# Kernel optimization log

Measured on AMD Instinct MI355X. Metric: run time of the kernel, lower is better.

Reference implementation:

```python
import jax, jax.numpy as jnp
import numpy as np

N, E, G = 50000, 800000, 128          # nodes, edges, graphs in batch
DF, DE, DT = 128, 256, 18             # dim_features, dim_embedding, dim_target
NUM_LAYERS = 4


def setup_inputs() -> dict:
    key = jax.random.key(0)
    ks = jax.random.split(key, 32)
    inp = {}
    inp["x"] = jax.random.normal(ks[0], (N, DF), jnp.float32)
    inp["edge_index"] = jax.random.randint(ks[1], (2, E), 0, N, dtype=jnp.int64)
    inp["batch"] = jnp.sort(jax.random.randint(ks[2], (N,), 0, G, dtype=jnp.int64))
    i = 3
    for l in range(NUM_LAYERS):
        din = DF if l == 0 else DE
        inp[f"Wl{l}"] = jax.random.normal(ks[i], (din, DE), jnp.float32) * (din ** -0.5); i += 1
        inp[f"bl{l}"] = jnp.zeros((DE,), jnp.float32)
        inp[f"Wr{l}"] = jax.random.normal(ks[i], (din, DE), jnp.float32) * (din ** -0.5); i += 1
        inp[f"Wm{l}"] = jax.random.normal(ks[i], (DE, DE), jnp.float32) * (DE ** -0.5); i += 1
        inp[f"bm{l}"] = jnp.zeros((DE,), jnp.float32)
    inp["fc1_W"] = jax.random.normal(ks[i], (NUM_LAYERS * DE, DE), jnp.float32) * ((NUM_LAYERS * DE) ** -0.5); i += 1
    inp["fc1_b"] = jnp.zeros((DE,), jnp.float32)
    inp["fc2_W"] = jax.random.normal(ks[i], (DE, DT), jnp.float32) * (DE ** -0.5); i += 1
    inp["fc2_b"] = jnp.zeros((DT,), jnp.float32)
    return inp


def _seg_max(v, idx, n):
    # scatter-max; empty segments -> 0 (PyG scatter 'max' convention)
    m = jax.ops.segment_max(v, idx, num_segments=n)
    return jnp.where(jnp.isfinite(m), m, 0.0)


def reference(x, edge_index, batch,
              Wl0, bl0, Wr0, Wm0, bm0,
              Wl1, bl1, Wr1, Wm1, bm1,
              Wl2, bl2, Wr2, Wm2, bm2,
              Wl3, bl3, Wr3, Wm3, bm3,
              fc1_W, fc1_b, fc2_W, fc2_b):
    src, dst = edge_index[0], edge_index[1]
    params = [(Wl0, bl0, Wr0, Wm0, bm0), (Wl1, bl1, Wr1, Wm1, bm1),
              (Wl2, bl2, Wr2, Wm2, bm2), (Wl3, bl3, Wr3, Wm3, bm3)]
    h = x
    outs = []
    for Wl, bl, Wr, Wm, bm in params:
        # SAGEConv(aggr='max'): lin_l(max_j x_j) + lin_r(x_i)
        agg = _seg_max(h[src], dst, h.shape[0])       # [N, din] gather + scatter-max
        h = agg @ Wl + bl + h @ Wr                    # [N, DE]
        h = jax.nn.relu(h @ Wm + bm)                  # fc_max + relu
        outs.append(h)
    hc = jnp.concatenate(outs, axis=1)                # [N, 4*DE]
    g = _seg_max(hc, batch, G)                        # global_max_pool -> [G, 4*DE]
    last_layer = jax.nn.relu(g @ fc1_W + fc1_b)       # [G, DE]
    out = last_layer @ fc2_W + fc2_b                  # [G, DT] (dropout = identity at eval)
    return jax.nn.log_softmax(out, axis=1), out, last_layer
```

## Files before the change

### kernel.cpp

```cpp
#include <hip/hip_runtime.h>
#include <stdint.h>

#define NN 50000
#define EE 800000
#define GG 128
#define DF 128
#define DE 256
#define NCHUNK ((NN + 255) / 256)

typedef unsigned short u16;
typedef __bf16 bf16x8 __attribute__((ext_vector_type(8)));
typedef float f32x4 __attribute__((ext_vector_type(4)));
typedef short s16x8 __attribute__((ext_vector_type(8)));

__device__ __forceinline__ float bf2f(u16 u) {
  union { unsigned int i; float f; } x; x.i = ((unsigned int)u) << 16; return x.f;
}
__device__ __forceinline__ u16 f2bf(float f) {
  union { float f; unsigned int i; } x; x.f = f;
  unsigned int i = x.i;
  return (u16)((i + 0x7fffu + ((i >> 16) & 1u)) >> 16);
}

__device__ __forceinline__ void async16(const void* g, void* l) {
  __builtin_amdgcn_global_load_lds(
      (const __attribute__((address_space(1))) void*)g,
      (__attribute__((address_space(3))) void*)l,
      16, 0, 0);
}

__device__ __forceinline__ s16x8 vmax8(s16x8 a, s16x8 b) {
  return __builtin_elementwise_max(a, b);
}

__global__ void detect_kernel(const u16* __restrict__ xr,
                              const unsigned* __restrict__ ei_words,
                              int* __restrict__ flags, int* __restrict__ counts) {
  int tid = threadIdx.x;
  if (blockIdx.x > 0) {
    int i = (blockIdx.x - 1) * 256 + tid;
    if (i < NN) counts[i] = 0;
    return;
  }
  __shared__ int red[2];
  if (tid < 2) red[tid] = 0;
  __syncthreads();
  int found = 0;
  for (int it = 0; it < 32; it++) {
    int i = it * 256 + tid;
    u16 a = xr[2 * i], b = xr[2 * i + 1];
    if (((a >> 7) & 0xFFu) == 0xFFu) found = 1;
    if (((b >> 7) & 0xFFu) == 0xFFu) found = 1;
  }
  if (__ballot(found)) { if ((tid & 63) == 0) atomicOr(&red[0], 1); }
  int nz = 0;
  if (tid < 128) {
    for (int j = 0; j < 4; j++) {
      unsigned w = ei_words[2 * (tid * 4 + j) + 1];
      if (w != 0u) nz = 1;
    }
  }
  if (__ballot(nz)) { if ((tid & 63) == 0) atomicOr(&red[1], 1); }
  __syncthreads();
  if (tid == 0) { flags[0] = red[0]; flags[1] = red[1]; }
}

__device__ __forceinline__ u16 ldw(const void* p, int idx, int f) {
  return f ? f2bf(((const float*)p)[idx]) : ((const u16*)p)[idx];
}

struct ConvSeg { const void* src; u16* dst; int start_blk; int n; };

struct PrepArgs {
  ConvSeg s[12]; int nseg; int conv_blocks;
  const void* x; u16* acat_x; u16* xk;
  const void* ei; const void* batch;
  int* src32; int* dst32; int* batch32; int* counts;
};

__global__ void prep_all(PrepArgs A, const int* __restrict__ flags) {
  int f = flags[0];
  int tid = threadIdx.x;
  int b = blockIdx.x;

  if (b < A.conv_blocks) {
    for (int i = 0; i < A.nseg; i++) {
      int nb = (A.s[i].n + 255) >> 8;
      if (b >= A.s[i].start_blk && b < A.s[i].start_blk + nb) {
        int idx = ((b - A.s[i].start_blk) << 8) + tid;
        if (idx < A.s[i].n) A.s[i].dst[idx] = ldw(A.s[i].src, idx, f);
        return;
      }
    }
    return;
  }
  b -= A.conv_blocks;

  if (b < 25000) {
    int i = b * 256 + tid;
    int node = i >> 7, d = i & 127;
    u16 v = ldw(A.x, i, f);
    A.acat_x[(long)node * 512 + d] = v;
    short s = (short)v;
    A.xk[i] = (u16)(s ^ ((s >> 15) & 0x7FFF));
    return;
  }
  b -= 25000;
  {
    int i64 = (flags[1] == 0);
    int i = b * 256 + tid;
    int s, d;
    if (i64) {
      s = (int)((const long long*)A.ei)[i];
      d = (int)((const long long*)A.ei)[EE + i];
    } else {
      s = ((const int*)A.ei)[i];
      d = ((const int*)A.ei)[EE + i];
    }
    s = min(max(s, 0), NN - 1);
    d = min(max(d, 0), NN - 1);
    A.src32[i] = s;
    A.dst32[i] = d;
    atomicAdd(&A.counts[d], 1);
    if (i < NN) {
      int bv = i64 ? (int)((const long long*)A.batch)[i] : ((const int*)A.batch)[i];
      A.batch32[i] = min(max(bv, 0), GG - 1);
    }
  }
}

struct TransArgs {
  const void* Wl[4]; const void* Wr[4]; const void* Wm[4]; const void* fc1W;
  u16* WcatT[4]; u16* WmT[4]; u16* fc1WT;
};

__global__ __launch_bounds__(256) void transpose_w(TransArgs T, const int* __restrict__ flags) {
  int f = flags[0];
  __shared__ u16 tile[64][65];
  int b = blockIdx.x;
  const void* src; u16* dst; int kt, ntile, Kd; int krow_off = 0;
  if (b < 16) {
    kt = b >> 2; ntile = b & 3; Kd = 256;
    if (kt * 64 < 128) { src = T.Wl[0]; } else { src = T.Wr[0]; krow_off = 128; }
    dst = T.WcatT[0];
  } else if (b < 112) {
    int l = 1 + (b - 16) / 32; int t = (b - 16) % 32;
    kt = t >> 2; ntile = t & 3; Kd = 512;
    if (kt * 64 < 256) { src = T.Wl[l]; } else { src = T.Wr[l]; krow_off = 256; }
    dst = T.WcatT[l];
  } else if (b < 176) {
    int l = (b - 112) / 16; int t = (b - 112) % 16;
    kt = t >> 2; ntile = t & 3; Kd = 256;
    src = T.Wm[l]; dst = T.WmT[l];
  } else {
    int t = b - 176;
    kt = t >> 2; ntile = t & 3; Kd = 1024;
    src = T.fc1W; dst = T.fc1WT;
  }
  int cj = threadIdx.x & 63, rp = threadIdx.x >> 6;
#pragma unroll 4
  for (int p = 0; p < 16; p++) {
    int krow = kt * 64 + p * 4 + rp;
    tile[p * 4 + rp][cj] = ldw(src, (krow - krow_off) * 256 + ntile * 64 + cj, f);
  }
  __syncthreads();
#pragma unroll 4
  for (int p = 0; p < 16; p++) {
    int nrow = ntile * 64 + p * 4 + rp;
    dst[(long)nrow * Kd + kt * 64 + cj] = tile[cj][p * 4 + rp];
  }
}

__global__ void rowptr_all(const int* __restrict__ counts, int* __restrict__ cursor,
                           int* __restrict__ row_ptr) {
  __shared__ int sh[256];
  int b = blockIdx.x, tid = threadIdx.x;
  int base = 0;
  for (int i = tid; i < b * 256; i += 256) base += counts[i];
  sh[tid] = base;
  __syncthreads();
  for (int off = 128; off > 0; off >>= 1) {
    if (tid < off) sh[tid] += sh[tid + off];
    __syncthreads();
  }
  base = sh[0];
  __syncthreads();
  int i = b * 256 + tid;
  int x = (i < NN) ? counts[i] : 0;
  sh[tid] = x;
  __syncthreads();
  for (int off = 1; off < 256; off <<= 1) {
    int v = (tid >= off) ? sh[tid - off] : 0;
    __syncthreads();
    sh[tid] += v;
    __syncthreads();
  }
  if (i < NN) {
    row_ptr[i + 1] = base + sh[tid];
    cursor[i] = base + sh[tid] - x;
  }
  if (i == 0) row_ptr[0] = 0;
}

__global__ void scatter_kernel(const int* __restrict__ srcA, const int* __restrict__ dstA,
                               int* __restrict__ cursor, int* __restrict__ col_src,
                               const int* __restrict__ batch, int* __restrict__ gs) {
  int e = blockIdx.x * blockDim.x + threadIdx.x;
  if (e < EE) {
    int slot = atomicAdd(&cursor[dstA[e]], 1);
    col_src[slot] = srcA[e];
  }
  if (blockIdx.x == 0 && threadIdx.x <= GG) {
    int g = threadIdx.x, lo = 0, hi = NN;
    while (lo < hi) { int mid = (lo + hi) >> 1; if (batch[mid] < g) lo = mid + 1; else hi = mid; }
    gs[g] = lo;
  }
}

template <int LPR, bool KEYED>
__global__ __launch_bounds__(256) void segmax_kernel(
    const u16* __restrict__ feat, int fstride,
    const int* __restrict__ row_ptr, const int* __restrict__ col_src,
    u16* __restrict__ agg_out, int ostride, int n) {
  constexpr int R = 64 / LPR;
  int node = blockIdx.x * 4 + (threadIdx.x >> 6);
  if (node >= n) return;
  int lane = threadIdx.x & 63;
  int sub = lane / LPR;
  int cp = lane % LPR;
  int beg = row_ptr[node], end = row_ptr[node + 1];
  s16x8 m = (s16x8)(short)(KEYED ? (short)0x807F : (short)0);
  const u16* fb = feat + cp * 8;

  int e = beg + sub;
  for (; e + 3 * R < end; e += 4 * R) {
    int s0 = col_src[e];
    int s1 = col_src[e + R];
    int s2 = col_src[e + 2 * R];
    int s3 = col_src[e + 3 * R];
    s16x8 v0 = *(const s16x8*)(fb + (long)s0 * fstride);
    s16x8 v1 = *(const s16x8*)(fb + (long)s1 * fstride);
    s16x8 v2 = *(const s16x8*)(fb + (long)s2 * fstride);
    s16x8 v3 = *(const s16x8*)(fb + (long)s3 * fstride);
    m = vmax8(m, vmax8(vmax8(v0, v1), vmax8(v2, v3)));
  }
  for (; e < end; e += R)
    m = vmax8(m, *(const s16x8*)(fb + (long)col_src[e] * fstride));

#pragma unroll
  for (int d = LPR; d < 64; d <<= 1) {
    union { s16x8 s; int i[4]; } t;
    t.s = m;
#pragma unroll
    for (int j = 0; j < 4; j++) t.i[j] = __shfl_xor(t.i[j], d);
    m = vmax8(m, t.s);
  }

  if (sub == 0) {
    if (KEYED) {
      if (beg == end) {
        m = (s16x8)(short)0;
      } else {
        s16x8 sp = (m >> 15) & (short)0x7FFF;
        m = m ^ sp;
      }
    }
    *(s16x8*)(agg_out + (long)node * ostride + cp * 8) = m;
  }
}

__global__ __launch_bounds__(512) void gemm256w(
    const u16* __restrict__ A, int lda, int K,
    const u16* __restrict__ BT,
    const u16* __restrict__ bias,
    u16* __restrict__ C, int ldc, int M, int relu_flag) {
  __shared__ u16 lsA[128 * 32];
  __shared__ u16 lsB[256 * 32];
  int tid = threadIdx.x;
  int lane = tid & 63, w = tid >> 6;
  int bm = blockIdx.x;
  int wm = (w & 1) << 6, wn = (w >> 1) << 6;
  int ln15 = lane & 15, quad = lane >> 4;

  f32x4 acc[4][4] = {};

  int r = tid >> 2;
  int c = (tid & 3) ^ (r & 3);
  const u16* gA = A + (long)min(bm * 128 + r, M - 1) * lda + c * 8;
  const u16* gB0 = BT + (long)r * K + c * 8;
  const u16* gB1 = BT + (long)(r + 128) * K + c * 8;
  u16* lA = lsA + w * 512;
  u16* lB0 = lsB + w * 512;
  u16* lB1 = lsB + 4096 + w * 512;
  int swz = (quad ^ (ln15 & 3)) << 3;

  for (int k0 = 0; k0 < K; k0 += 32) {
    async16(gA + k0, lA);
    async16(gB0 + k0, lB0);
    async16(gB1 + k0, lB1);
    __syncthreads();
    bf16x8 af[4], bfr[4];
#pragma unroll
    for (int t = 0; t < 4; t++) {
      af[t]  = *(const bf16x8*)(lsA + (wm + t * 16 + ln15) * 32 + swz);
      bfr[t] = *(const bf16x8*)(lsB + (wn + t * 16 + ln15) * 32 + swz);
    }
#pragma unroll
    for (int mt = 0; mt < 4; mt++)
#pragma unroll
      for (int nt = 0; nt < 4; nt++)
        acc[mt][nt] = __builtin_amdgcn_mfma_f32_16x16x32_bf16(af[mt], bfr[nt], acc[mt][nt], 0, 0, 0);
    __syncthreads();
  }

  float bv[4];
#pragma unroll
  for (int nt = 0; nt < 4; nt++)
    bv[nt] = bf2f(bias[wn + nt * 16 + ln15]);

#pragma unroll
  for (int mt = 0; mt < 4; mt++) {
    int row0 = bm * 128 + wm + mt * 16 + quad * 4;
#pragma unroll
    for (int rr = 0; rr < 4; rr++) {
      int row = row0 + rr;
      if (row < M) {
#pragma unroll
        for (int nt = 0; nt < 4; nt++) {
          float v = acc[mt][nt][rr] + bv[nt];
          if (relu_flag) v = fmaxf(v, 0.f);
          C[(long)row * ldc + wn + nt * 16 + ln15] = f2bf(v);
        }
      }
    }
  }
}

__global__ void pool_kernel(const u16* __restrict__ h, const int* __restrict__ gs,
                            u16* __restrict__ g_pool, int l) {
  int g = blockIdx.x;
  int chunk = threadIdx.x & 31;
  int rg = threadIdx.x >> 5;
  int beg = gs[g], end = gs[g + 1];
  s16x8 m = (s16x8)(short)0;
  const u16* hp = h + chunk * 8;
  for (int n = beg + rg; n < end; n += 32)
    m = vmax8(m, *(const s16x8*)(hp + (long)n * 512));
  __shared__ s16x8 red[32][32];
  red[rg][chunk] = m;
  __syncthreads();
  for (int s = 16; s >= 1; s >>= 1) {
    if (rg < s) red[rg][chunk] = vmax8(red[rg][chunk], red[rg + s][chunk]);
    __syncthreads();
  }
  if (rg == 0)
    *(s16x8*)(g_pool + g * 1024 + l * 256 + chunk * 8) = red[0][chunk];
}

__global__ __launch_bounds__(256) void fc1_gemm(
    const u16* __restrict__ A,
    const u16* __restrict__ BT,
    float* __restrict__ Cpart) {
  __shared__ u16 lsA[128 * 32];
  __shared__ u16 lsB[128 * 32];
  int tid = threadIdx.x;
  int lane = tid & 63, w = tid >> 6;
  int slice = blockIdx.x >> 1, bn = blockIdx.x & 1;
  int wm = (w & 1) << 6, wn = (w >> 1) << 6;
  int ln15 = lane & 15, quad = lane >> 4;

  f32x4 acc[4][4] = {};

  int cm = lane >> 2;
  int ck = (lane & 3) << 3;
  int kb = slice * 256;

  const u16* gA0 = A + (long)(w * 16 + cm) * 1024 + kb + ck;
  const u16* gA1 = A + (long)((w + 4) * 16 + cm) * 1024 + kb + ck;
  const u16* gB0 = BT + (long)(bn * 128 + w * 16 + cm) * 1024 + kb + ck;
  const u16* gB1 = BT + (long)(bn * 128 + (w + 4) * 16 + cm) * 1024 + kb + ck;
  u16* lA0 = lsA + w * 512;
  u16* lA1 = lsA + (w + 4) * 512;
  u16* lB0 = lsB + w * 512;
  u16* lB1 = lsB + (w + 4) * 512;

  for (int k0 = 0; k0 < 256; k0 += 32) {
    async16(gA0 + k0, lA0);
    async16(gA1 + k0, lA1);
    async16(gB0 + k0, lB0);
    async16(gB1 + k0, lB1);
    __syncthreads();
    bf16x8 af[4], bfr[4];
#pragma unroll
    for (int t = 0; t < 4; t++) {
      af[t]  = *(const bf16x8*)(lsA + (wm + t * 16 + ln15) * 32 + quad * 8);
      bfr[t] = *(const bf16x8*)(lsB + (wn + t * 16 + ln15) * 32 + quad * 8);
    }
#pragma unroll
    for (int mt = 0; mt < 4; mt++)
#pragma unroll
      for (int nt = 0; nt < 4; nt++)
        acc[mt][nt] = __builtin_amdgcn_mfma_f32_16x16x32_bf16(af[mt], bfr[nt], acc[mt][nt], 0, 0, 0);
    __syncthreads();
  }

  float* Cb = Cpart + slice * (GG * 256);
#pragma unroll
  for (int mt = 0; mt < 4; mt++) {
    int row0 = wm + mt * 16 + quad * 4;
#pragma unroll
    for (int r = 0; r < 4; r++)
#pragma unroll
      for (int nt = 0; nt < 4; nt++)
        Cb[(row0 + r) * 256 + bn * 128 + wn + nt * 16 + ln15] = acc[mt][nt][r];
  }
}

__global__ void fc2_head(const float* __restrict__ fc1part,
                         const u16* __restrict__ fc1b,
                         const u16* __restrict__ W,
                         const u16* __restrict__ b,
                         void* __restrict__ outbuf, const int* __restrict__ flags) {
  int g = blockIdx.x, t = threadIdx.x;
  __shared__ float lr[256];
  __shared__ float ps[144];
  __shared__ float sv[18];
  __shared__ float sred[2];
  float v = bf2f(fc1b[t]);
#pragma unroll
  for (int s = 0; s < 4; s++) v += fc1part[s * (GG * 256) + g * 256 + t];
  v = fmaxf(v, 0.f);
  lr[t] = v;
  if (flags[0]) ((float*)outbuf)[4608 + g * 256 + t] = v;
  else          ((u16*)outbuf)[4608 + g * 256 + t] = f2bf(v);
  __syncthreads();
  if (t < 144) {
    int o = t % 18, s = t / 18;
    float acc = 0.f;
    int k0 = s * 32;
#pragma unroll 8
    for (int k = k0; k < k0 + 32; k++)
      acc += lr[k] * bf2f(W[k * 18 + o]);
    ps[t] = acc;
  }
  __syncthreads();
  if (t < 18) {
    float acc = bf2f(b[t]);
#pragma unroll
    for (int s = 0; s < 8; s++) acc += ps[s * 18 + t];
    sv[t] = acc;
  }
  __syncthreads();
  if (t == 0) {
    float mx = sv[0];
    for (int i = 1; i < 18; i++) mx = fmaxf(mx, sv[i]);
    float s = 0.f;
    for (int i = 0; i < 18; i++) s += expf(sv[i] - mx);
    sred[0] = mx; sred[1] = logf(s);
  }
  __syncthreads();
  if (t < 18) {
    float raw = sv[t];
    float lsm = raw - sred[0] - sred[1];
    if (flags[0]) {
      ((float*)outbuf)[g * 18 + t] = lsm;
      ((float*)outbuf)[2304 + g * 18 + t] = raw;
    } else {
      ((u16*)outbuf)[g * 18 + t] = f2bf(lsm);
      ((u16*)outbuf)[2304 + g * 18 + t] = f2bf(raw);
    }
  }
}

extern "C" void kernel_launch(void* const* d_in, const int* in_sizes, int n_in,
                              void* d_out, int out_size, void* d_ws, size_t ws_size,
                              hipStream_t stream) {
  (void)in_sizes; (void)n_in; (void)out_size; (void)ws_size;
  const void* x = d_in[0];
  const void* ei = d_in[1];
  const void* batch = d_in[2];
  const void *Wl[4], *bl[4], *Wr[4], *Wm[4], *bm[4];
  for (int l = 0; l < 4; l++) {
    Wl[l] = d_in[3 + l * 5 + 0];
    bl[l] = d_in[3 + l * 5 + 1];
    Wr[l] = d_in[3 + l * 5 + 2];
    Wm[l] = d_in[3 + l * 5 + 3];
    bm[l] = d_in[3 + l * 5 + 4];
  }
  const void* fc1W = d_in[23];
  const void* fc1b = d_in[24];
  const void* fc2W = d_in[25];
  const void* fc2b = d_in[26];

  char* ws = (char*)d_ws;
  size_t off = 0;
  auto alloc = [&](size_t bytes) -> void* {
    void* p = ws + off;
    off = (off + bytes + 255) & ~(size_t)255;
    return p;
  };
  int* flags   = (int*)alloc(16);
  int* row_ptr = (int*)alloc((NN + 1) * sizeof(int));
  int* counts  = (int*)alloc(NN * sizeof(int));
  int* cursor  = (int*)alloc(NN * sizeof(int));
  int* col_src = (int*)alloc((size_t)EE * sizeof(int));
  int* src32   = (int*)alloc((size_t)EE * sizeof(int));
  int* dst32   = (int*)alloc((size_t)EE * sizeof(int));
  int* batch32 = (int*)alloc(NN * sizeof(int));
  int* gs      = (int*)alloc((GG + 1) * sizeof(int));
  u16* WcatT[4]; for (int l = 0; l < 4; l++) WcatT[l] = (u16*)alloc(256 * 512 * 2);
  u16* WmT[4];   for (int l = 0; l < 4; l++) WmT[l]   = (u16*)alloc(256 * 256 * 2);
  u16* bl_bf[4]; for (int l = 0; l < 4; l++) bl_bf[l] = (u16*)alloc(256 * 2);
  u16* bm_bf[4]; for (int l = 0; l < 4; l++) bm_bf[l] = (u16*)alloc(256 * 2);
  u16* fc1WT   = (u16*)alloc(256 * 1024 * 2);
  u16* fc1b_bf = (u16*)alloc(256 * 2);
  u16* fc2W_bf = (u16*)alloc(256 * 18 * 2);
  u16* fc2b_bf = (u16*)alloc(18 * 2);
  u16* xk      = (u16*)alloc((size_t)NN * DF * 2);
  u16* Acat    = (u16*)alloc((size_t)NN * 512 * 2);
  u16* tmp     = (u16*)alloc((size_t)NN * 256 * 2);
  u16* gpool   = (u16*)alloc(GG * 1024 * 2);
  float* fc1part = (float*)alloc(4 * GG * 256 * sizeof(float));

  detect_kernel<<<1 + NCHUNK, 256, 0, stream>>>((const u16*)x, (const unsigned*)ei, flags, counts);

  TransArgs TA;
  for (int l = 0; l < 4; l++) {
    TA.Wl[l] = Wl[l]; TA.Wr[l] = Wr[l]; TA.Wm[l] = Wm[l];
    TA.WcatT[l] = WcatT[l]; TA.WmT[l] = WmT[l];
  }
  TA.fc1W = fc1W; TA.fc1WT = fc1WT;
  transpose_w<<<240, 256, 0, stream>>>(TA, flags);

  PrepArgs PA;
  int blk = 0, si = 0;
  auto addseg = [&](const void* s, u16* d, int n) {
    PA.s[si].src = s; PA.s[si].dst = d; PA.s[si].start_blk = blk; PA.s[si].n = n;
    blk += (n + 255) / 256; si++;
  };
  addseg(fc2W, fc2W_bf, 256 * 18);
  for (int l = 0; l < 4; l++) addseg(bl[l], bl_bf[l], 256);
  for (int l = 0; l < 4; l++) addseg(bm[l], bm_bf[l], 256);
  addseg(fc1b, fc1b_bf, 256);
  addseg(fc2b, fc2b_bf, 18);
  PA.nseg = si; PA.conv_blocks = blk;
  PA.x = x; PA.acat_x = Acat + DF; PA.xk = xk;
  PA.ei = ei; PA.batch = batch;
  PA.src32 = src32; PA.dst32 = dst32; PA.batch32 = batch32; PA.counts = counts;
  prep_all<<<PA.conv_blocks + 25000 + 3125, 256, 0, stream>>>(PA, flags);

  rowptr_all<<<NCHUNK, 256, 0, stream>>>(counts, cursor, row_ptr);
  scatter_kernel<<<(EE + 255) / 256, 256, 0, stream>>>(src32, dst32, cursor, col_src, batch32, gs);

  int segblocks = (NN + 3) / 4;
  int gemmgrid = (NN + 127) / 128;

  for (int l = 0; l < 4; l++) {
    if (l == 0) {
      segmax_kernel<16, true><<<segblocks, 256, 0, stream>>>(xk, DF, row_ptr, col_src,
                                                             Acat, 512, NN);
    } else {
      segmax_kernel<32, false><<<segblocks, 256, 0, stream>>>(Acat + 256, 512, row_ptr, col_src,
                                                              Acat, 512, NN);
    }
    int K = (l == 0) ? 256 : 512;
    gemm256w<<<gemmgrid, 512, 0, stream>>>(Acat, 512, K, WcatT[l], bl_bf[l], tmp, 256, NN, 0);
    gemm256w<<<gemmgrid, 512, 0, stream>>>(tmp, 256, 256, WmT[l], bm_bf[l], Acat + 256, 512, NN, 1);
    pool_kernel<<<GG, 1024, 0, stream>>>(Acat + 256, gs, gpool, l);
  }

  fc1_gemm<<<8, 256, 0, stream>>>(gpool, fc1WT, fc1part);
  fc2_head<<<GG, 256, 0, stream>>>(fc1part, fc1b_bf, fc2W_bf, fc2b_bf, d_out, flags);
}
```

Baseline: 622.2 us.

## Build CSR with two-level bucket sort instead of global atomics

Replaces per-node global atomic counting, a quadratic-ish prefix scan and atomic scatter with a two-pass bucket sort. Edges are first binned into 196 buckets of 256 destination nodes, with counts kept in shared memory, then each bucket is sorted locally in LDS to produce row_ptr and col_src. This cuts global atomic contention and the expensive rowptr scan, which re-summed counts per block. It adds an extra pass and an 800K-word intermediate buffer, and the order of edges within a row is still nondeterministic.

Result: faster. 560.6 us (-9.9%).

```diff
diff --git a/kernel.cpp b/kernel.cpp
--- a/kernel.cpp
+++ b/kernel.cpp
@@ -6,7 +6,7 @@
 #define GG 128
 #define DF 128
 #define DE 256
-#define NCHUNK ((NN + 255) / 256)
+#define NB 196
 
 typedef unsigned short u16;
 typedef __bf16 bf16x8 __attribute__((ext_vector_type(8)));
@@ -35,11 +35,10 @@
 
 __global__ void detect_kernel(const u16* __restrict__ xr,
                               const unsigned* __restrict__ ei_words,
-                              int* __restrict__ flags, int* __restrict__ counts) {
+                              int* __restrict__ flags, int* __restrict__ bucket_cnt) {
   int tid = threadIdx.x;
-  if (blockIdx.x > 0) {
-    int i = (blockIdx.x - 1) * 256 + tid;
-    if (i < NN) counts[i] = 0;
+  if (blockIdx.x == 1) {
+    if (tid < NB) bucket_cnt[tid] = 0;
     return;
   }
   __shared__ int red[2];
@@ -75,7 +74,7 @@
   ConvSeg s[12]; int nseg; int conv_blocks;
   const void* x; u16* acat_x; u16* xk;
   const void* ei; const void* batch;
-  int* src32; int* dst32; int* batch32; int* counts;
+  int* src32; int* dst32; int* batch32; int* bucket_cnt;
 };
 
 __global__ void prep_all(PrepArgs A, const int* __restrict__ flags) {
@@ -106,27 +105,36 @@
     return;
   }
   b -= 25000;
-  {
-    int i64 = (flags[1] == 0);
-    int i = b * 256 + tid;
-    int s, d;
-    if (i64) {
-      s = (int)((const long long*)A.ei)[i];
-      d = (int)((const long long*)A.ei)[EE + i];
-    } else {
-      s = ((const int*)A.ei)[i];
-      d = ((const int*)A.ei)[EE + i];
-    }
-    s = min(max(s, 0), NN - 1);
-    d = min(max(d, 0), NN - 1);
-    A.src32[i] = s;
-    A.dst32[i] = d;
-    atomicAdd(&A.counts[d], 1);
+
+  __shared__ int h[NB];
+  if (tid < NB) h[tid] = 0;
+  __syncthreads();
+  int i64 = (flags[1] == 0);
+  int e0 = b * 2048;
+  for (int j = 0; j < 8; j++) {
+    int i = e0 + j * 256 + tid;
+    if (i < EE) {
+      int s, d;
+      if (i64) {
+        s = (int)((const long long*)A.ei)[i];
+        d = (int)((const long long*)A.ei)[EE + i];
+      } else {
+        s = ((const int*)A.ei)[i];
+        d = ((const int*)A.ei)[EE + i];
+      }
+      s = min(max(s, 0), NN - 1);
+      d = min(max(d, 0), NN - 1);
+      A.src32[i] = s;
+      A.dst32[i] = d;
+      atomicAdd(&h[d >> 8], 1);
+    }
     if (i < NN) {
       int bv = i64 ? (int)((const long long*)A.batch)[i] : ((const int*)A.batch)[i];
       A.batch32[i] = min(max(bv, 0), GG - 1);
     }
   }
+  __syncthreads();
+  if (tid < NB) atomicAdd(&A.bucket_cnt[tid], h[tid]);
 }
 
 struct TransArgs {
@@ -171,22 +179,12 @@
   }
 }
 
-__global__ void rowptr_all(const int* __restrict__ counts, int* __restrict__ cursor,
-                           int* __restrict__ row_ptr) {
+__global__ void bucket_scan(const int* __restrict__ bucket_cnt, int* __restrict__ bucket_base,
+                            int* __restrict__ bucket_cur,
+                            const int* __restrict__ batch, int* __restrict__ gs) {
   __shared__ int sh[256];
-  int b = blockIdx.x, tid = threadIdx.x;
-  int base = 0;
-  for (int i = tid; i < b * 256; i += 256) base += counts[i];
-  sh[tid] = base;
-  __syncthreads();
-  for (int off = 128; off > 0; off >>= 1) {
-    if (tid < off) sh[tid] += sh[tid + off];
-    __syncthreads();
-  }
-  base = sh[0];
-  __syncthreads();
-  int i = b * 256 + tid;
-  int x = (i < NN) ? counts[i] : 0;
+  int tid = threadIdx.x;
+  int x = (tid < NB) ? bucket_cnt[tid] : 0;
   sh[tid] = x;
   __syncthreads();
   for (int off = 1; off < 256; off <<= 1) {
@@ -195,26 +193,76 @@
     sh[tid] += v;
     __syncthreads();
   }
-  if (i < NN) {
-    row_ptr[i + 1] = base + sh[tid];
-    cursor[i] = base + sh[tid] - x;
-  }
-  if (i == 0) row_ptr[0] = 0;
-}
-
-__global__ void scatter_kernel(const int* __restrict__ srcA, const int* __restrict__ dstA,
-                               int* __restrict__ cursor, int* __restrict__ col_src,
-                               const int* __restrict__ batch, int* __restrict__ gs) {
-  int e = blockIdx.x * blockDim.x + threadIdx.x;
-  if (e < EE) {
-    int slot = atomicAdd(&cursor[dstA[e]], 1);
-    col_src[slot] = srcA[e];
-  }
-  if (blockIdx.x == 0 && threadIdx.x <= GG) {
-    int g = threadIdx.x, lo = 0, hi = NN;
+  if (tid < NB) { bucket_base[tid] = sh[tid] - x; bucket_cur[tid] = sh[tid] - x; }
+  if (tid == 0) bucket_base[NB] = EE;
+  if (tid <= GG) {
+    int g = tid, lo = 0, hi = NN;
     while (lo < hi) { int mid = (lo + hi) >> 1; if (batch[mid] < g) lo = mid + 1; else hi = mid; }
     gs[g] = lo;
   }
+}
+
+__global__ __launch_bounds__(256) void bucket_pass1(
+    const int* __restrict__ src32, const int* __restrict__ dst32,
+    int* __restrict__ bucket_cur, unsigned* __restrict__ bucket_buf) {
+  __shared__ int lcnt[NB];
+  __shared__ int lbase[NB];
+  int tid = threadIdx.x, b = blockIdx.x;
+  if (tid < NB) lcnt[tid] = 0;
+  __syncthreads();
+  int e0 = b * 2048;
+  int lofs[8]; unsigned pk[8]; int bk[8];
+#pragma unroll
+  for (int j = 0; j < 8; j++) {
+    int i = e0 + j * 256 + tid;
+    if (i < EE) {
+      int s = src32[i], d = dst32[i];
+      bk[j] = d >> 8;
+      pk[j] = ((unsigned)s << 8) | (unsigned)(d & 255);
+      lofs[j] = atomicAdd(&lcnt[bk[j]], 1);
+    } else bk[j] = -1;
+  }
+  __syncthreads();
+  if (tid < NB) lbase[tid] = atomicAdd(&bucket_cur[tid], lcnt[tid]);
+  __syncthreads();
+#pragma unroll
+  for (int j = 0; j < 8; j++)
+    if (bk[j] >= 0)
+      bucket_buf[lbase[bk[j]] + lofs[j]] = pk[j];
+}
+
+__global__ __launch_bounds__(256) void bucket_pass2(
+    const unsigned* __restrict__ bucket_buf, const int* __restrict__ bucket_base,
+    int* __restrict__ col_src, int* __restrict__ row_ptr) {
+  __shared__ int cnt[256];
+  __shared__ int sh[256];
+  __shared__ int cur[256];
+  int tid = threadIdx.x, b = blockIdx.x;
+  int ebase = bucket_base[b], eend = bucket_base[b + 1];
+  cnt[tid] = 0;
+  __syncthreads();
+  for (int e = ebase + tid; e < eend; e += 256)
+    atomicAdd(&cnt[bucket_buf[e] & 255u], 1);
+  __syncthreads();
+  int x = cnt[tid];
+  sh[tid] = x;
+  __syncthreads();
+  for (int off = 1; off < 256; off <<= 1) {
+    int v = (tid >= off) ? sh[tid - off] : 0;
+    __syncthreads();
+    sh[tid] += v;
+    __syncthreads();
+  }
+  int node = b * 256 + tid;
+  if (node < NN) row_ptr[node + 1] = ebase + sh[tid];
+  cur[tid] = ebase + sh[tid] - x;
+  __syncthreads();
+  for (int e = ebase + tid; e < eend; e += 256) {
+    unsigned p = bucket_buf[e];
+    int slot = atomicAdd(&cur[p & 255u], 1);
+    col_src[slot] = (int)(p >> 8);
+  }
+  if (b == 0 && tid == 0) row_ptr[0] = 0;
 }
 
 template <int LPR, bool KEYED>
@@ -499,10 +547,12 @@
     off = (off + bytes + 255) & ~(size_t)255;
     return p;
   };
-  int* flags   = (int*)alloc(16);
-  int* row_ptr = (int*)alloc((NN + 1) * sizeof(int));
-  int* counts  = (int*)alloc(NN * sizeof(int));
-  int* cursor  = (int*)alloc(NN * sizeof(int));
+  int* flags       = (int*)alloc(16);
+  int* row_ptr     = (int*)alloc((NN + 1) * sizeof(int));
+  int* bucket_cnt  = (int*)alloc(NB * sizeof(int));
+  int* bucket_base = (int*)alloc((NB + 1) * sizeof(int));
+  int* bucket_cur  = (int*)alloc(NB * sizeof(int));
+  unsigned* bucket_buf = (unsigned*)alloc((size_t)EE * sizeof(unsigned));
   int* col_src = (int*)alloc((size_t)EE * sizeof(int));
   int* src32   = (int*)alloc((size_t)EE * sizeof(int));
   int* dst32   = (int*)alloc((size_t)EE * sizeof(int));
@@ -522,7 +572,7 @@
   u16* gpool   = (u16*)alloc(GG * 1024 * 2);
   float* fc1part = (float*)alloc(4 * GG * 256 * sizeof(float));
 
-  detect_kernel<<<1 + NCHUNK, 256, 0, stream>>>((const u16*)x, (const unsigned*)ei, flags, counts);
+  detect_kernel<<<2, 256, 0, stream>>>((const u16*)x, (const unsigned*)ei, flags, bucket_cnt);
 
   TransArgs TA;
   for (int l = 0; l < 4; l++) {
@@ -546,11 +596,12 @@
   PA.nseg = si; PA.conv_blocks = blk;
   PA.x = x; PA.acat_x = Acat + DF; PA.xk = xk;
   PA.ei = ei; PA.batch = batch;
-  PA.src32 = src32; PA.dst32 = dst32; PA.batch32 = batch32; PA.counts = counts;
-  prep_all<<<PA.conv_blocks + 25000 + 3125, 256, 0, stream>>>(PA, flags);
-
-  rowptr_all<<<NCHUNK, 256, 0, stream>>>(counts, cursor, row_ptr);
-  scatter_kernel<<<(EE + 255) / 256, 256, 0, stream>>>(src32, dst32, cursor, col_src, batch32, gs);
+  PA.src32 = src32; PA.dst32 = dst32; PA.batch32 = batch32; PA.bucket_cnt = bucket_cnt;
+  prep_all<<<PA.conv_blocks + 25000 + 391, 256, 0, stream>>>(PA, flags);
+
+  bucket_scan<<<1, 256, 0, stream>>>(bucket_cnt, bucket_base, bucket_cur, batch32, gs);
+  bucket_pass1<<<391, 256, 0, stream>>>(src32, dst32, bucket_cur, bucket_buf);
+  bucket_pass2<<<NB, 256, 0, stream>>>(bucket_buf, bucket_base, col_src, row_ptr);
 
   int segblocks = (NN + 3) / 4;
   int gemmgrid = (NN + 127) / 128;
```
